# Kernel tuning notes

Hardware: AMD Instinct MI355X
Metric: run time of the kernel (lower is better)

Reference implementation:

```python
import jax, jax.numpy as jnp
import numpy as np

H = 512          # hidden_size
DEPTH = 6        # number of tanh layers
N = 8192         # collocation points
DT = 0.1         # uniform time step
MIN_ALPHA = 0.6  # initial_params['min_alpha']


def _xavier(k, fi, fo):
    lim = np.sqrt(6.0 / (fi + fo))
    return jax.random.uniform(k, (fi, fo), minval=-lim, maxval=lim, dtype=jnp.float32)


def _raw(x):
    # inverse-softplus style init used by EpiPINN: raw = x + log(-expm1(-x))
    return jnp.array([x + np.log(-np.expm1(-x))], dtype=jnp.float32)


def setup_inputs() -> dict:
    key = jax.random.key(0)
    ks = jax.random.split(key, DEPTH + 2)
    W_in = _xavier(ks[0], 1, H)
    b_in = jnp.zeros((H,), jnp.float32)
    Wh = jnp.stack([_xavier(ks[1 + l], H, H) for l in range(DEPTH - 1)])  # [DEPTH-1,H,H]
    bh = jnp.zeros((DEPTH - 1, H), jnp.float32)
    W_out = _xavier(ks[DEPTH], H, 5)
    b_out = jnp.zeros((5,), jnp.float32)
    t = (jnp.arange(N, dtype=jnp.float32) * DT).reshape(N, 1)
    return {
        't': t,
        'W_in': W_in, 'b_in': b_in, 'Wh': Wh, 'bh': bh,
        'W_out': W_out, 'b_out': b_out,
        'raw_beta': _raw(0.3), 'raw_sigma': _raw(0.2),
        'raw_gamma': _raw(0.1), 'raw_mu': _raw(0.05),
        'z_alpha': jnp.array([0.0], dtype=jnp.float32),
    }


def _forward_all(t, W_in, b_in, Wh, bh, W_out, b_out,
                 raw_beta, raw_sigma, raw_gamma, raw_mu, z_alpha):
    # --- PINN MLP: 1 -> H (tanh) x DEPTH -> 5, softmax over components ---
    h = jnp.tanh(t @ W_in + b_in)
    for l in range(Wh.shape[0]):  # static small loop over layers
        h = jnp.tanh(h @ Wh[l] + bh[l])
    y = jax.nn.softmax(h @ W_out + b_out, axis=1)  # [n,5]

    alpha = MIN_ALPHA + (1.0 - MIN_ALPHA) * jax.nn.sigmoid(z_alpha[0])
    beta = jax.nn.softplus(raw_beta[0])
    sigma = jax.nn.softplus(raw_sigma[0])
    gamma = jax.nn.softplus(raw_gamma[0])
    mu = jax.nn.softplus(raw_mu[0])

    # --- Caputo L1 fractional derivative for all 5 components at once ---
    n = y.shape[0]
    dpsi = y[1:] - y[:-1]  # [n-1,5] first differences
    rs = jnp.arange(n - 1, dtype=y.dtype)
    rs_safe = jnp.where(rs == 0, 1.0, rs)  # avoid 0**x grad nan; value unchanged
    ws = (rs + 1.0) ** (1.0 - alpha) - jnp.where(rs == 0, 0.0, rs_safe ** (1.0 - alpha))
    C = DT ** (-alpha) / jnp.exp(jax.lax.lgamma(2.0 - alpha))
    ii = jnp.arange(n - 1)
    idx = ii[:, None] - ii[None, :]
    A = jnp.where(idx >= 0, ws[jnp.clip(idx, 0)], 0.0)  # lower-triangular Toeplitz [n-1,n-1]
    dfrac = jnp.concatenate([jnp.zeros((1, 5), y.dtype), C * (A @ dpsi)], axis=0)  # [n,5]

    # --- SEIRD right-hand side and physics residual ---
    s, e, i, r, d = (y[:, k:k + 1] for k in range(5))
    living = 1.0 - d
    inf_term = beta * s * i / living
    f = jnp.concatenate([
        -inf_term,
        inf_term - sigma * e,
        sigma * e - (gamma + mu) * i,
        gamma * i,
        mu * i,
    ], axis=1)  # [n,5]
    return jnp.mean((dfrac - f) ** 2)


def reference(t, W_in, b_in, Wh, bh, W_out, b_out,
              raw_beta, raw_sigma, raw_gamma, raw_mu, z_alpha):
    return _forward_all(t, W_in, b_in, Wh, bh, W_out, b_out,
                        raw_beta, raw_sigma, raw_gamma, raw_mu, z_alpha)
```

## Files before the change

### kernel.cpp

```cpp
#include <hip/hip_runtime.h>
#include <math.h>

typedef short short8v __attribute__((ext_vector_type(8)));
typedef float float4v __attribute__((ext_vector_type(4)));

#define N_PTS 8192
#define HDIM  512
#define NHID  5
#define KSTR  1024
#define NCH   16

#define OFF_XA    0ull
#define OFF_XB    16777216ull
#define OFF_WT    33554432ull
#define OFF_Y     38797312ull
#define OFF_DPSI  38961152ull
#define OFF_WSW   39124992ull
#define OFF_PART  39157760ull
#define OFF_BPART 41779200ull

__device__ __forceinline__ unsigned short f2bf(float x) {
  unsigned u = __builtin_bit_cast(unsigned, x);
  u += 0x7FFFu + ((u >> 16) & 1u);
  return (unsigned short)(u >> 16);
}
__device__ __forceinline__ float bf2f(unsigned short h) {
  unsigned u = ((unsigned)h) << 16;
  return __builtin_bit_cast(float, u);
}

#define GLOAD16(gsrc, ldst) \
  __builtin_amdgcn_global_load_lds( \
      (const __attribute__((address_space(1))) void*)(gsrc), \
      (__attribute__((address_space(3))) void*)(ldst), 16, 0, 0)

__global__ void wprep_kernel(const float* __restrict__ Wh,
                             unsigned short* __restrict__ WT) {
  __shared__ float tile[32][33];
  int l = blockIdx.z;
  int kb = blockIdx.x;
  int n0 = blockIdx.y * 32;
  int j = threadIdx.x & 31, i8 = threadIdx.x >> 5;
  const float* W = Wh + (size_t)l * HDIM * HDIM;
#pragma unroll
  for (int q = 0; q < 4; ++q)
    tile[i8 + 8 * q][j] = W[(size_t)(kb * 32 + i8 + 8 * q) * HDIM + n0 + j];
  __syncthreads();
#pragma unroll
  for (int q = 0; q < 4; ++q) {
    int n = n0 + i8 + 8 * q;
    float v = tile[j][i8 + 8 * q];
    unsigned short h = f2bf(v);
    unsigned short lo = f2bf(v - bf2f(h));
    size_t o = ((size_t)l * HDIM + n) * KSTR + kb * 64 + j;
    WT[o] = h; WT[o + 32] = lo;
  }
}

__global__ void layer0_kernel(const float* __restrict__ t,
                              const float* __restrict__ Win,
                              const float* __restrict__ bin,
                              unsigned short* __restrict__ X) {
  int gid = blockIdx.x * blockDim.x + threadIdx.x;
  int row = gid >> 7;
  int jq  = (gid & 127) << 2;
  float tv = t[row];
  float4 w = *(const float4*)(Win + jq);
  float4 b = *(const float4*)(bin + jq);
  float v[4];
  v[0] = tanhf(tv * w.x + b.x); v[1] = tanhf(tv * w.y + b.y);
  v[2] = tanhf(tv * w.z + b.z); v[3] = tanhf(tv * w.w + b.w);
  ushort4 h4, l4;
  h4.x = f2bf(v[0]); l4.x = f2bf(v[0] - bf2f(h4.x));
  h4.y = f2bf(v[1]); l4.y = f2bf(v[1] - bf2f(h4.y));
  h4.z = f2bf(v[2]); l4.z = f2bf(v[2] - bf2f(h4.z));
  h4.w = f2bf(v[3]); l4.w = f2bf(v[3] - bf2f(h4.w));
  size_t o = (size_t)row * KSTR + (jq >> 5) * 64 + (jq & 31);
  *(ushort4*)(X + o) = h4;
  *(ushort4*)(X + o + 32) = l4;
}

__global__ __launch_bounds__(256) void gemm_split_kernel(
    const unsigned short* __restrict__ A,
    const unsigned short* __restrict__ Bt,
    const float* __restrict__ bias,
    unsigned short* __restrict__ C) {
  __shared__ __align__(16) short lds[3][12288];
  const int tid = threadIdx.x;
  const int lane = tid & 63, w = tid >> 6;
  const int wc = w;
  const int r0 = blockIdx.x * 64, c0 = blockIdx.y * 128;
  const int rl = lane & 15, kgrp = lane >> 4;

  float4v acc[4][2];
#pragma unroll
  for (int i = 0; i < 4; ++i)
#pragma unroll
    for (int j = 0; j < 2; ++j) acc[i][j] = (float4v){0.f, 0.f, 0.f, 0.f};

  auto stage = [&](int b, int kt) {
    const int kbase = kt * 64;
#pragma unroll
    for (int i = 0; i < 2; ++i) {
      int c = i * 256 + tid;
      int row = c >> 3, m = c & 7;
      int gs = m ^ (row & 7);
      GLOAD16(A + (size_t)(r0 + row) * KSTR + kbase + gs * 8,
              &lds[b][(i * 256 + w * 64) * 8]);
    }
#pragma unroll
    for (int i = 0; i < 4; ++i) {
      int c = i * 256 + tid;
      int col = c >> 3, m = c & 7;
      int gs = m ^ (col & 7);
      GLOAD16(Bt + (size_t)(c0 + col) * KSTR + kbase + gs * 8,
              &lds[b][4096 + (i * 256 + w * 64) * 8]);
    }
  };

  stage(0, 0);
  stage(1, 1);
  asm volatile("s_waitcnt vmcnt(6)" ::: "memory");
  __builtin_amdgcn_s_barrier();
  asm volatile("" ::: "memory");

#pragma unroll 1
  for (int kt = 0; kt < 16; ++kt) {
    if (kt < 14) stage((kt + 2) % 3, kt + 2);
    const short* bufc = lds[kt % 3];
    short8v ahi[4], alo[4], bhi[2], blo[2];
#pragma unroll
    for (int mi = 0; mi < 4; ++mi) {
      int row = mi * 16 + rl;
      int sh = kgrp ^ (row & 7);
      int sl = (kgrp + 4) ^ (row & 7);
      ahi[mi] = *(const short8v*)&bufc[row * 64 + sh * 8];
      alo[mi] = *(const short8v*)&bufc[row * 64 + sl * 8];
    }
#pragma unroll
    for (int ni = 0; ni < 2; ++ni) {
      int col = wc * 32 + ni * 16 + rl;
      int sh = kgrp ^ (col & 7);
      int sl = (kgrp + 4) ^ (col & 7);
      bhi[ni] = *(const short8v*)&bufc[4096 + col * 64 + sh * 8];
      blo[ni] = *(const short8v*)&bufc[4096 + col * 64 + sl * 8];
    }
    __builtin_amdgcn_s_setprio(1);
#pragma unroll
    for (int mi = 0; mi < 4; ++mi)
#pragma unroll
      for (int ni = 0; ni < 2; ++ni)
        acc[mi][ni] = __builtin_amdgcn_mfma_f32_16x16x32_bf16(ahi[mi], bhi[ni], acc[mi][ni], 0, 0, 0);
#pragma unroll
    for (int mi = 0; mi < 4; ++mi)
#pragma unroll
      for (int ni = 0; ni < 2; ++ni)
        acc[mi][ni] = __builtin_amdgcn_mfma_f32_16x16x32_bf16(ahi[mi], blo[ni], acc[mi][ni], 0, 0, 0);
#pragma unroll
    for (int mi = 0; mi < 4; ++mi)
#pragma unroll
      for (int ni = 0; ni < 2; ++ni)
        acc[mi][ni] = __builtin_amdgcn_mfma_f32_16x16x32_bf16(alo[mi], bhi[ni], acc[mi][ni], 0, 0, 0);
    __builtin_amdgcn_s_setprio(0);
    if (kt < 15) {
      if (kt < 14) asm volatile("s_waitcnt vmcnt(6)" ::: "memory");
      else         asm volatile("s_waitcnt vmcnt(0)" ::: "memory");
      __builtin_amdgcn_s_barrier();
      asm volatile("" ::: "memory");
    }
  }

  float bcol[2];
#pragma unroll
  for (int ni = 0; ni < 2; ++ni) bcol[ni] = bias[c0 + wc * 32 + ni * 16 + rl];
#pragma unroll
  for (int mi = 0; mi < 4; ++mi)
#pragma unroll
    for (int ni = 0; ni < 2; ++ni)
#pragma unroll
      for (int r = 0; r < 4; ++r) {
        int row = r0 + mi * 16 + kgrp * 4 + r;
        int col = c0 + wc * 32 + ni * 16 + rl;
        float v = tanhf(acc[mi][ni][r] + bcol[ni]);
        unsigned short h = f2bf(v);
        unsigned short lo = f2bf(v - bf2f(h));
        size_t o = (size_t)row * KSTR + (col >> 5) * 64 + (col & 31);
        C[o] = h; C[o + 32] = lo;
      }
}

__global__ void outlayer_kernel(const unsigned short* __restrict__ X,
                                const float* __restrict__ Wout,
                                const float* __restrict__ bout,
                                float* __restrict__ y) {
  int wid  = threadIdx.x >> 6;
  int lane = threadIdx.x & 63;
  int row  = blockIdx.x * 4 + wid;
  size_t o = (size_t)row * KSTR + (lane >> 2) * 64 + (lane & 3) * 8;
  short8v hv = *(const short8v*)(X + o);
  short8v lv = *(const short8v*)(X + o + 32);
  const float* wrp = Wout + lane * 40;
  float acc[5] = {0.f, 0.f, 0.f, 0.f, 0.f};
#pragma unroll
  for (int e = 0; e < 8; ++e) {
    float h = bf2f((unsigned short)hv[e]) + bf2f((unsigned short)lv[e]);
#pragma unroll
    for (int c = 0; c < 5; ++c) acc[c] += h * wrp[e * 5 + c];
  }
#pragma unroll
  for (int c = 0; c < 5; ++c)
    for (int off = 32; off; off >>= 1) acc[c] += __shfl_down(acc[c], off);
  if (lane == 0) {
    float l[5], m = -1e30f;
#pragma unroll
    for (int c = 0; c < 5; ++c) { l[c] = acc[c] + bout[c]; m = fmaxf(m, l[c]); }
    float s = 0.f;
#pragma unroll
    for (int c = 0; c < 5; ++c) { l[c] = expf(l[c] - m); s += l[c]; }
    float inv = 1.f / s;
#pragma unroll
    for (int c = 0; c < 5; ++c) y[row * 5 + c] = l[c] * inv;
  }
}

__global__ void prep_caputo_kernel(const float* __restrict__ z_alpha,
                                   const float* __restrict__ y,
                                   float* __restrict__ wsw,
                                   float* __restrict__ dpsi) {
  int g = blockIdx.x * blockDim.x + threadIdx.x;
  if (g < (N_PTS - 1) * 5) dpsi[g] = y[g + 5] - y[g];
  if (g < N_PTS - 1) {
    double z = (double)z_alpha[0];
    double alpha = 0.6 + 0.4 / (1.0 + exp(-z));
    double p = 1.0 - alpha;
    double w = pow((double)g + 1.0, p) - (g == 0 ? 0.0 : pow((double)g, p));
    wsw[g] = (float)w;
  }
}

__global__ __launch_bounds__(256) void conv_kernel(
    const float* __restrict__ dpsi, const float* __restrict__ wsw,
    float* __restrict__ part) {
  __shared__ float dps[256][8];
  __shared__ float wsl[512];
  int tid = threadIdx.x;
  int r0  = blockIdx.x * 256;
  int ch  = blockIdx.y;
  int r   = r0 + tid;
  float acc[5] = {0.f, 0.f, 0.f, 0.f, 0.f};

  for (int t4 = 0; t4 < 2; ++t4) {
    int j0 = ch * 512 + t4 * 256;
    if (j0 > r0 + 254) break;
    __syncthreads();
    {
      const float* dr = dpsi + (size_t)(j0 + tid) * 5;
      dps[tid][0] = dr[0]; dps[tid][1] = dr[1]; dps[tid][2] = dr[2];
      dps[tid][3] = dr[3]; dps[tid][4] = dr[4];
    }
    int base = r0 - j0 - 256;
#pragma unroll
    for (int s = 0; s < 2; ++s) {
      int i = tid + s * 256;
      int src = base + i;
      wsl[i] = (src >= 0 && src < N_PTS - 1) ? wsw[src] : 0.f;
    }
    __syncthreads();
    int widx = tid + 255;
#pragma unroll 4
    for (int jj = 0; jj < 256; ++jj) {
      float w = wsl[widx - jj];
      float4 d4 = *(const float4*)&dps[jj][0];
      float d5 = dps[jj][4];
      acc[0] += w * d4.x; acc[1] += w * d4.y; acc[2] += w * d4.z;
      acc[3] += w * d4.w; acc[4] += w * d5;
    }
  }
  float* p = part + ((size_t)ch * N_PTS + r) * 5;
  p[0] = acc[0]; p[1] = acc[1]; p[2] = acc[2]; p[3] = acc[3]; p[4] = acc[4];
}

__device__ __forceinline__ float softplusf_(float x) {
  return x > 20.f ? x : log1pf(expf(x));
}

__global__ void combine_kernel(const float* __restrict__ y,
                               const float* __restrict__ part,
                               const float* __restrict__ rb, const float* __restrict__ rs,
                               const float* __restrict__ rg, const float* __restrict__ rm,
                               const float* __restrict__ za,
                               float* __restrict__ bpart) {
  __shared__ float red[128];
  int tid = threadIdx.x;
  int row = blockIdx.x * 128 + tid;

  float beta  = softplusf_(rb[0]);
  float sigma = softplusf_(rs[0]);
  float gamma = softplusf_(rg[0]);
  float mu    = softplusf_(rm[0]);
  double z = (double)za[0];
  double alpha = 0.6 + 0.4 / (1.0 + exp(-z));
  float C = (float)(pow(0.1, -alpha) / tgamma(2.0 - alpha));

  float df[5];
  if (row == 0) {
    df[0] = df[1] = df[2] = df[3] = df[4] = 0.f;
  } else {
#pragma unroll
    for (int c = 0; c < 5; ++c) {
      float s = 0.f;
#pragma unroll
      for (int ch = 0; ch < NCH; ++ch)
        s += part[((size_t)ch * N_PTS + row) * 5 + c];
      df[c] = C * s;
    }
  }
  float yv[5];
#pragma unroll
  for (int c = 0; c < 5; ++c) yv[c] = y[row * 5 + c];
  float living = 1.f - yv[4];
  float inf_t = beta * yv[0] * yv[2] / living;
  float f[5];
  f[0] = -inf_t;
  f[1] = inf_t - sigma * yv[1];
  f[2] = sigma * yv[1] - (gamma + mu) * yv[2];
  f[3] = gamma * yv[2];
  f[4] = mu * yv[2];
  float s = 0.f;
#pragma unroll
  for (int c = 0; c < 5; ++c) { float d = df[c] - f[c]; s += d * d; }

  red[tid] = s;
  __syncthreads();
  for (int off = 64; off; off >>= 1) {
    if (tid < off) red[tid] += red[tid + off];
    __syncthreads();
  }
  if (tid == 0) bpart[blockIdx.x] = red[0];
}

__global__ void finish_kernel(const float* __restrict__ bpart, float* __restrict__ out) {
  if (threadIdx.x == 0) {
    float s = 0.f;
    for (int i = 0; i < 64; ++i) s += bpart[i];
    out[0] = s / (float)(N_PTS * 5);
  }
}

extern "C" void kernel_launch(void* const* d_in, const int* in_sizes, int n_in,
                              void* d_out, int out_size, void* d_ws, size_t ws_size,
                              hipStream_t stream) {
  const float* t     = (const float*)d_in[0];
  const float* W_in  = (const float*)d_in[1];
  const float* b_in  = (const float*)d_in[2];
  const float* Wh    = (const float*)d_in[3];
  const float* bh    = (const float*)d_in[4];
  const float* W_out = (const float*)d_in[5];
  const float* b_out = (const float*)d_in[6];
  const float* rbta  = (const float*)d_in[7];
  const float* rsig  = (const float*)d_in[8];
  const float* rgam  = (const float*)d_in[9];
  const float* rmu   = (const float*)d_in[10];
  const float* zalp  = (const float*)d_in[11];

  char* wsb = (char*)d_ws;
  unsigned short* XA = (unsigned short*)(wsb + OFF_XA);
  unsigned short* XB = (unsigned short*)(wsb + OFF_XB);
  unsigned short* WT = (unsigned short*)(wsb + OFF_WT);
  float* y     = (float*)(wsb + OFF_Y);
  float* dpsi  = (float*)(wsb + OFF_DPSI);
  float* wsw   = (float*)(wsb + OFF_WSW);
  float* part  = (float*)(wsb + OFF_PART);
  float* bpart = (float*)(wsb + OFF_BPART);
  float* out   = (float*)d_out;

  wprep_kernel<<<dim3(16, 16, 5), 256, 0, stream>>>(Wh, WT);

  layer0_kernel<<<N_PTS * 128 / 256, 256, 0, stream>>>(t, W_in, b_in, XA);

  for (int l = 0; l < NHID; ++l) {
    const unsigned short* in = (l & 1) ? XB : XA;
    unsigned short*      oub = (l & 1) ? XA : XB;
    gemm_split_kernel<<<dim3(N_PTS / 64, HDIM / 128), 256, 0, stream>>>(
        in, WT + (size_t)l * HDIM * KSTR, bh + (size_t)l * HDIM, oub);
  }

  outlayer_kernel<<<N_PTS / 4, 256, 0, stream>>>(XB, W_out, b_out, y);

  prep_caputo_kernel<<<160, 256, 0, stream>>>(zalp, y, wsw, dpsi);

  conv_kernel<<<dim3(N_PTS / 256, NCH), 256, 0, stream>>>(dpsi, wsw, part);

  combine_kernel<<<N_PTS / 128, 128, 0, stream>>>(y, part, rbta, rsig, rgam, rmu,
                                                  zalp, bpart);
  finish_kernel<<<1, 64, 0, stream>>>(bpart, out);
  (void)in_sizes; (void)n_in; (void)out_size; (void)ws_size;
}
```

Measured before the change: 138.6 us.

## Fuse whole MLP into one kernel keeping activations resident in LDS

Replaces the layer0 kernel, five split-bf16 GEMM launches and the output-layer kernel with one kernel. Each 512-thread block owns 32 rows and keeps their hi/lo bf16 activations in a 64 KB swizzled LDS buffer across all layers. Weights are streamed directly from global memory into registers with double buffering. This removes the large global activation round-trips and the extra launches, but it loses the LDS-staged weight reuse and gives only 256 blocks with large LDS use, so occupancy is low and weight reads from L2 are repeated for every block.

```diff
diff --git a/kernel.cpp b/kernel.cpp
--- a/kernel.cpp
+++ b/kernel.cpp
@@ -10,8 +10,6 @@
 #define KSTR  1024
 #define NCH   16
 
-#define OFF_XA    0ull
-#define OFF_XB    16777216ull
 #define OFF_WT    33554432ull
 #define OFF_Y     38797312ull
 #define OFF_DPSI  38961152ull
@@ -28,11 +26,6 @@
   unsigned u = ((unsigned)h) << 16;
   return __builtin_bit_cast(float, u);
 }
-
-#define GLOAD16(gsrc, ldst) \
-  __builtin_amdgcn_global_load_lds( \
-      (const __attribute__((address_space(1))) void*)(gsrc), \
-      (__attribute__((address_space(3))) void*)(ldst), 16, 0, 0)
 
 __global__ void wprep_kernel(const float* __restrict__ Wh,
                              unsigned short* __restrict__ WT) {
@@ -57,170 +50,160 @@
   }
 }
 
-__global__ void layer0_kernel(const float* __restrict__ t,
-                              const float* __restrict__ Win,
-                              const float* __restrict__ bin,
-                              unsigned short* __restrict__ X) {
-  int gid = blockIdx.x * blockDim.x + threadIdx.x;
-  int row = gid >> 7;
-  int jq  = (gid & 127) << 2;
-  float tv = t[row];
-  float4 w = *(const float4*)(Win + jq);
-  float4 b = *(const float4*)(bin + jq);
-  float v[4];
-  v[0] = tanhf(tv * w.x + b.x); v[1] = tanhf(tv * w.y + b.y);
-  v[2] = tanhf(tv * w.z + b.z); v[3] = tanhf(tv * w.w + b.w);
-  ushort4 h4, l4;
-  h4.x = f2bf(v[0]); l4.x = f2bf(v[0] - bf2f(h4.x));
-  h4.y = f2bf(v[1]); l4.y = f2bf(v[1] - bf2f(h4.y));
-  h4.z = f2bf(v[2]); l4.z = f2bf(v[2] - bf2f(h4.z));
-  h4.w = f2bf(v[3]); l4.w = f2bf(v[3] - bf2f(h4.w));
-  size_t o = (size_t)row * KSTR + (jq >> 5) * 64 + (jq & 31);
-  *(ushort4*)(X + o) = h4;
-  *(ushort4*)(X + o + 32) = l4;
-}
-
-__global__ __launch_bounds__(256) void gemm_split_kernel(
-    const unsigned short* __restrict__ A,
-    const unsigned short* __restrict__ Bt,
-    const float* __restrict__ bias,
-    unsigned short* __restrict__ C) {
-  __shared__ __align__(16) short lds[3][12288];
-  const int tid = threadIdx.x;
+__global__ __launch_bounds__(512) void mlp_fused_kernel(
+    const float* __restrict__ t,
+    const float* __restrict__ Win, const float* __restrict__ bin,
+    const unsigned short* __restrict__ WT,
+    const float* __restrict__ bh,
+    const float* __restrict__ Wout, const float* __restrict__ bout,
+    float* __restrict__ y) {
+  __shared__ __align__(16) unsigned short act[32 * 1024];
+  const int tid  = threadIdx.x;
   const int lane = tid & 63, w = tid >> 6;
-  const int wc = w;
-  const int r0 = blockIdx.x * 64, c0 = blockIdx.y * 128;
-  const int rl = lane & 15, kgrp = lane >> 4;
-
-  float4v acc[4][2];
-#pragma unroll
-  for (int i = 0; i < 4; ++i)
-#pragma unroll
-    for (int j = 0; j < 2; ++j) acc[i][j] = (float4v){0.f, 0.f, 0.f, 0.f};
-
-  auto stage = [&](int b, int kt) {
-    const int kbase = kt * 64;
-#pragma unroll
-    for (int i = 0; i < 2; ++i) {
-      int c = i * 256 + tid;
-      int row = c >> 3, m = c & 7;
-      int gs = m ^ (row & 7);
-      GLOAD16(A + (size_t)(r0 + row) * KSTR + kbase + gs * 8,
-              &lds[b][(i * 256 + w * 64) * 8]);
-    }
-#pragma unroll
-    for (int i = 0; i < 4; ++i) {
-      int c = i * 256 + tid;
-      int col = c >> 3, m = c & 7;
-      int gs = m ^ (col & 7);
-      GLOAD16(Bt + (size_t)(c0 + col) * KSTR + kbase + gs * 8,
-              &lds[b][4096 + (i * 256 + w * 64) * 8]);
-    }
-  };
-
-  stage(0, 0);
-  stage(1, 1);
-  asm volatile("s_waitcnt vmcnt(6)" ::: "memory");
-  __builtin_amdgcn_s_barrier();
-  asm volatile("" ::: "memory");
+  const int rl   = lane & 15, kgrp = lane >> 4;
+  const int r0   = blockIdx.x * 32;
+  const int cb   = w * 64;
+
+  {
+    int row = tid >> 4;
+    int kb  = tid & 15;
+    float tv = t[r0 + row];
+    int m = row & 7;
+#pragma unroll
+    for (int p = 0; p < 32; ++p) {
+      int col = kb * 32 + p;
+      float v = tanhf(tv * Win[col] + bin[col]);
+      unsigned short h = f2bf(v);
+      unsigned short lo = f2bf(v - bf2f(h));
+      act[row * 1024 + kb * 64 + (((p >> 3) ^ m) * 8) + (p & 7)] = h;
+      act[row * 1024 + kb * 64 + ((((p >> 3) | 4) ^ m) * 8) + (p & 7)] = lo;
+    }
+  }
+  __syncthreads();
+
+  int aoff_h[2], aoff_l[2];
+#pragma unroll
+  for (int mi = 0; mi < 2; ++mi) {
+    int row = mi * 16 + rl;
+    aoff_h[mi] = row * 1024 + (kgrp ^ (row & 7)) * 8;
+    aoff_l[mi] = row * 1024 + ((kgrp + 4) ^ (row & 7)) * 8;
+  }
+
+#define LOADB(BH, BL, KB)                                            \
+  do {                                                               \
+    _Pragma("unroll")                                                \
+    for (int ni = 0; ni < 4; ++ni) {                                 \
+      BH[ni] = *(const short8v*)(bp[ni] + (KB) * 64);                \
+      BL[ni] = *(const short8v*)(bp[ni] + (KB) * 64 + 32);           \
+    }                                                                \
+  } while (0)
+
+#define COMPUTE(KB, BH, BL)                                          \
+  do {                                                               \
+    short8v ah[2], al[2];                                            \
+    _Pragma("unroll")                                                \
+    for (int mi = 0; mi < 2; ++mi) {                                 \
+      ah[mi] = *(const short8v*)&act[aoff_h[mi] + (KB) * 64];        \
+      al[mi] = *(const short8v*)&act[aoff_l[mi] + (KB) * 64];        \
+    }                                                                \
+    _Pragma("unroll")                                                \
+    for (int mi = 0; mi < 2; ++mi)                                   \
+      _Pragma("unroll")                                              \
+      for (int ni = 0; ni < 4; ++ni)                                 \
+        acc[mi][ni] = __builtin_amdgcn_mfma_f32_16x16x32_bf16(       \
+            ah[mi], BH[ni], acc[mi][ni], 0, 0, 0);                   \
+    _Pragma("unroll")                                                \
+    for (int mi = 0; mi < 2; ++mi)                                   \
+      _Pragma("unroll")                                              \
+      for (int ni = 0; ni < 4; ++ni)                                 \
+        acc[mi][ni] = __builtin_amdgcn_mfma_f32_16x16x32_bf16(       \
+            ah[mi], BL[ni], acc[mi][ni], 0, 0, 0);                   \
+    _Pragma("unroll")                                                \
+    for (int mi = 0; mi < 2; ++mi)                                   \
+      _Pragma("unroll")                                              \
+      for (int ni = 0; ni < 4; ++ni)                                 \
+        acc[mi][ni] = __builtin_amdgcn_mfma_f32_16x16x32_bf16(       \
+            al[mi], BH[ni], acc[mi][ni], 0, 0, 0);                   \
+  } while (0)
+
+  for (int l = 0; l < NHID; ++l) {
+    const unsigned short* Wl = WT + (size_t)l * HDIM * KSTR;
+    const float* bias = bh + l * HDIM;
+
+    const unsigned short* bp[4];
+#pragma unroll
+    for (int ni = 0; ni < 4; ++ni)
+      bp[ni] = Wl + (size_t)(cb + ni * 16 + rl) * KSTR + kgrp * 8;
+
+    float4v acc[2][4];
+#pragma unroll
+    for (int mi = 0; mi < 2; ++mi)
+#pragma unroll
+      for (int ni = 0; ni < 4; ++ni) acc[mi][ni] = (float4v){0.f, 0.f, 0.f, 0.f};
+
+    short8v bhc[4], blc[4], bhn[4], bln[4];
+    LOADB(bhc, blc, 0);
+    for (int kb = 0; kb < 16; kb += 2) {
+      LOADB(bhn, bln, kb + 1);
+      COMPUTE(kb, bhc, blc);
+      if (kb + 2 < 16) LOADB(bhc, blc, kb + 2);
+      COMPUTE(kb + 1, bhn, bln);
+    }
+
+    __syncthreads();
+    float bcol[4];
+#pragma unroll
+    for (int ni = 0; ni < 4; ++ni) bcol[ni] = bias[cb + ni * 16 + rl];
+#pragma unroll
+    for (int mi = 0; mi < 2; ++mi)
+#pragma unroll
+      for (int ni = 0; ni < 4; ++ni)
+#pragma unroll
+        for (int r = 0; r < 4; ++r) {
+          int row = mi * 16 + kgrp * 4 + r;
+          int col = cb + ni * 16 + rl;
+          float v = tanhf(acc[mi][ni][r] + bcol[ni]);
+          unsigned short h = f2bf(v);
+          unsigned short lo = f2bf(v - bf2f(h));
+          int kb2 = col >> 5, pos = col & 31, m = row & 7;
+          act[row * 1024 + kb2 * 64 + (((pos >> 3) ^ m) * 8) + (pos & 7)] = h;
+          act[row * 1024 + kb2 * 64 + ((((pos >> 3) | 4) ^ m) * 8) + (pos & 7)] = lo;
+        }
+    __syncthreads();
+  }
 
 #pragma unroll 1
-  for (int kt = 0; kt < 16; ++kt) {
-    if (kt < 14) stage((kt + 2) % 3, kt + 2);
-    const short* bufc = lds[kt % 3];
-    short8v ahi[4], alo[4], bhi[2], blo[2];
-#pragma unroll
-    for (int mi = 0; mi < 4; ++mi) {
-      int row = mi * 16 + rl;
-      int sh = kgrp ^ (row & 7);
-      int sl = (kgrp + 4) ^ (row & 7);
-      ahi[mi] = *(const short8v*)&bufc[row * 64 + sh * 8];
-      alo[mi] = *(const short8v*)&bufc[row * 64 + sl * 8];
-    }
-#pragma unroll
-    for (int ni = 0; ni < 2; ++ni) {
-      int col = wc * 32 + ni * 16 + rl;
-      int sh = kgrp ^ (col & 7);
-      int sl = (kgrp + 4) ^ (col & 7);
-      bhi[ni] = *(const short8v*)&bufc[4096 + col * 64 + sh * 8];
-      blo[ni] = *(const short8v*)&bufc[4096 + col * 64 + sl * 8];
-    }
-    __builtin_amdgcn_s_setprio(1);
-#pragma unroll
-    for (int mi = 0; mi < 4; ++mi)
-#pragma unroll
-      for (int ni = 0; ni < 2; ++ni)
-        acc[mi][ni] = __builtin_amdgcn_mfma_f32_16x16x32_bf16(ahi[mi], bhi[ni], acc[mi][ni], 0, 0, 0);
-#pragma unroll
-    for (int mi = 0; mi < 4; ++mi)
-#pragma unroll
-      for (int ni = 0; ni < 2; ++ni)
-        acc[mi][ni] = __builtin_amdgcn_mfma_f32_16x16x32_bf16(ahi[mi], blo[ni], acc[mi][ni], 0, 0, 0);
-#pragma unroll
-    for (int mi = 0; mi < 4; ++mi)
-#pragma unroll
-      for (int ni = 0; ni < 2; ++ni)
-        acc[mi][ni] = __builtin_amdgcn_mfma_f32_16x16x32_bf16(alo[mi], bhi[ni], acc[mi][ni], 0, 0, 0);
-    __builtin_amdgcn_s_setprio(0);
-    if (kt < 15) {
-      if (kt < 14) asm volatile("s_waitcnt vmcnt(6)" ::: "memory");
-      else         asm volatile("s_waitcnt vmcnt(0)" ::: "memory");
-      __builtin_amdgcn_s_barrier();
-      asm volatile("" ::: "memory");
-    }
-  }
-
-  float bcol[2];
-#pragma unroll
-  for (int ni = 0; ni < 2; ++ni) bcol[ni] = bias[c0 + wc * 32 + ni * 16 + rl];
-#pragma unroll
-  for (int mi = 0; mi < 4; ++mi)
-#pragma unroll
-    for (int ni = 0; ni < 2; ++ni)
-#pragma unroll
-      for (int r = 0; r < 4; ++r) {
-        int row = r0 + mi * 16 + kgrp * 4 + r;
-        int col = c0 + wc * 32 + ni * 16 + rl;
-        float v = tanhf(acc[mi][ni][r] + bcol[ni]);
-        unsigned short h = f2bf(v);
-        unsigned short lo = f2bf(v - bf2f(h));
-        size_t o = (size_t)row * KSTR + (col >> 5) * 64 + (col & 31);
-        C[o] = h; C[o + 32] = lo;
-      }
-}
-
-__global__ void outlayer_kernel(const unsigned short* __restrict__ X,
-                                const float* __restrict__ Wout,
-                                const float* __restrict__ bout,
-                                float* __restrict__ y) {
-  int wid  = threadIdx.x >> 6;
-  int lane = threadIdx.x & 63;
-  int row  = blockIdx.x * 4 + wid;
-  size_t o = (size_t)row * KSTR + (lane >> 2) * 64 + (lane & 3) * 8;
-  short8v hv = *(const short8v*)(X + o);
-  short8v lv = *(const short8v*)(X + o + 32);
-  const float* wrp = Wout + lane * 40;
-  float acc[5] = {0.f, 0.f, 0.f, 0.f, 0.f};
-#pragma unroll
-  for (int e = 0; e < 8; ++e) {
-    float h = bf2f((unsigned short)hv[e]) + bf2f((unsigned short)lv[e]);
-#pragma unroll
-    for (int c = 0; c < 5; ++c) acc[c] += h * wrp[e * 5 + c];
-  }
-#pragma unroll
-  for (int c = 0; c < 5; ++c)
-    for (int off = 32; off; off >>= 1) acc[c] += __shfl_down(acc[c], off);
-  if (lane == 0) {
-    float l[5], m = -1e30f;
-#pragma unroll
-    for (int c = 0; c < 5; ++c) { l[c] = acc[c] + bout[c]; m = fmaxf(m, l[c]); }
-    float s = 0.f;
-#pragma unroll
-    for (int c = 0; c < 5; ++c) { l[c] = expf(l[c] - m); s += l[c]; }
-    float inv = 1.f / s;
-#pragma unroll
-    for (int c = 0; c < 5; ++c) y[row * 5 + c] = l[c] * inv;
-  }
+  for (int rr = 0; rr < 4; ++rr) {
+    int row = w * 4 + rr;
+    int m = row & 7;
+    int kb = lane >> 2, pg = lane & 3;
+    short8v hv = *(const short8v*)&act[row * 1024 + kb * 64 + ((pg ^ m) * 8)];
+    short8v lv = *(const short8v*)&act[row * 1024 + kb * 64 + (((pg | 4) ^ m) * 8)];
+    const float* wrp = Wout + lane * 40;
+    float a5[5] = {0.f, 0.f, 0.f, 0.f, 0.f};
+#pragma unroll
+    for (int e = 0; e < 8; ++e) {
+      float h = bf2f((unsigned short)hv[e]) + bf2f((unsigned short)lv[e]);
+#pragma unroll
+      for (int c = 0; c < 5; ++c) a5[c] += h * wrp[e * 5 + c];
+    }
+#pragma unroll
+    for (int c = 0; c < 5; ++c)
+      for (int off = 32; off; off >>= 1) a5[c] += __shfl_down(a5[c], off);
+    if (lane == 0) {
+      float lg[5], mx = -1e30f;
+#pragma unroll
+      for (int c = 0; c < 5; ++c) { lg[c] = a5[c] + bout[c]; mx = fmaxf(mx, lg[c]); }
+      float s = 0.f;
+#pragma unroll
+      for (int c = 0; c < 5; ++c) { lg[c] = expf(lg[c] - mx); s += lg[c]; }
+      float inv = 1.f / s;
+#pragma unroll
+      for (int c = 0; c < 5; ++c) y[(r0 + row) * 5 + c] = lg[c] * inv;
+    }
+  }
+#undef LOADB
+#undef COMPUTE
 }
 
 __global__ void prep_caputo_kernel(const float* __restrict__ z_alpha,
@@ -364,8 +347,6 @@
   const float* zalp  = (const float*)d_in[11];
 
   char* wsb = (char*)d_ws;
-  unsigned short* XA = (unsigned short*)(wsb + OFF_XA);
-  unsigned short* XB = (unsigned short*)(wsb + OFF_XB);
   unsigned short* WT = (unsigned short*)(wsb + OFF_WT);
   float* y     = (float*)(wsb + OFF_Y);
   float* dpsi  = (float*)(wsb + OFF_DPSI);
@@ -376,16 +357,8 @@
 
   wprep_kernel<<<dim3(16, 16, 5), 256, 0, stream>>>(Wh, WT);
 
-  layer0_kernel<<<N_PTS * 128 / 256, 256, 0, stream>>>(t, W_in, b_in, XA);
-
-  for (int l = 0; l < NHID; ++l) {
-    const unsigned short* in = (l & 1) ? XB : XA;
-    unsigned short*      oub = (l & 1) ? XA : XB;
-    gemm_split_kernel<<<dim3(N_PTS / 64, HDIM / 128), 256, 0, stream>>>(
-        in, WT + (size_t)l * HDIM * KSTR, bh + (size_t)l * HDIM, oub);
-  }
-
-  outlayer_kernel<<<N_PTS / 4, 256, 0, stream>>>(XB, W_out, b_out, y);
+  mlp_fused_kernel<<<N_PTS / 32, 512, 0, stream>>>(
+      t, W_in, b_in, WT, bh, W_out, b_out, y);
 
   prep_caputo_kernel<<<160, 256, 0, stream>>>(zalp, y, wsw, dpsi);
 
```

New measurement: 219.9 us. +58.6%, slower.
